# Optimization experiments

Measured on AMD Instinct MI355X. Metric: run time of the kernel, lower is better.

Reference implementation:

```python
import jax, jax.numpy as jnp
import numpy as np

T, B = 512, 256
OBS, ACT, HID, HF = 128, 32, 512, 512
IN = OBS + ACT  # GRUCell input: stoch_dim + action_dim
LOG2PI = float(np.log(2.0 * np.pi))


def _lin(key, out_f, in_f):
    k1, k2 = jax.random.split(key)
    s = 1.0 / np.sqrt(in_f)
    w = jax.random.uniform(k1, (out_f, in_f), jnp.float32, -s, s)
    b = jax.random.uniform(k2, (out_f,), jnp.float32, -s, s)
    return w, b


def setup_inputs() -> dict:
    key = jax.random.key(0)
    ks = jax.random.split(key, 16)
    obs = jax.random.normal(ks[0], (T, B, OBS), jnp.float32)
    action = jax.random.normal(ks[1], (T, B, ACT), jnp.float32)
    reward = jax.random.normal(ks[2], (T, B, 1), jnp.float32)
    w_ih, b_ih = _lin(ks[3], 3 * HID, IN)
    w_hh, b_hh = _lin(ks[4], 3 * HID, HID)
    ow0, ob0 = _lin(ks[5], HF, HID); ow1, ob1 = _lin(ks[6], HF, HF); ow2, ob2 = _lin(ks[7], OBS, HF)
    aw0, ab0 = _lin(ks[8], HF, HID); aw1, ab1 = _lin(ks[9], HF, HF); aw2, ab2 = _lin(ks[10], ACT, HF)
    rw0, rb0 = _lin(ks[11], HF, HID); rw1, rb1 = _lin(ks[12], HF, HF); rw2, rb2 = _lin(ks[13], 1, HF)
    return dict(obs=obs, action=action, reward=reward,
                w_ih=w_ih, w_hh=w_hh, b_ih=b_ih, b_hh=b_hh,
                ow0=ow0, ob0=ob0, ow1=ow1, ob1=ob1, ow2=ow2, ob2=ob2,
                aw0=aw0, ab0=ab0, aw1=aw1, ab1=ab1, aw2=aw2, ab2=ab2,
                rw0=rw0, rb0=rb0, rw1=rw1, rb1=rb1, rw2=rw2, rb2=rb2)


def _gru(x, h, w_ih, w_hh, b_ih, b_hh):
    # PyTorch GRUCell math
    gi = x @ w_ih.T + b_ih
    gh = h @ w_hh.T + b_hh
    ir, iz, inn = jnp.split(gi, 3, axis=-1)
    hr, hz, hn = jnp.split(gh, 3, axis=-1)
    r = jax.nn.sigmoid(ir + hr)
    z = jax.nn.sigmoid(iz + hz)
    n = jnp.tanh(inn + r * hn)
    return (1.0 - z) * n + z * h


def _mlp(x, w0, b0, w1, b1, w2, b2):
    x = jax.nn.elu(x @ w0.T + b0)
    x = jax.nn.elu(x @ w1.T + b1)
    return x @ w2.T + b2


def _logprob(x, mu):
    # Normal(mu, 1).log_prob(x)
    return -0.5 * (x - mu) ** 2 - 0.5 * LOG2PI


def reference(obs, action, reward,
              w_ih, w_hh, b_ih, b_hh,
              ow0, ob0, ow1, ob1, ow2, ob2,
              aw0, ab0, aw1, ab1, aw2, ab2,
              rw0, rb0, rw1, rb1, rw2, rb2):
    # initial h: GRUCell(cat([obs[0], zeros]), h=0)
    x0 = jnp.concatenate([obs[0], jnp.zeros_like(action[0])], axis=-1)
    h0 = _gru(x0, jnp.zeros((B, HID), obs.dtype), w_ih, w_hh, b_ih, b_hh)
    xseq = jnp.concatenate([obs, action], axis=-1)  # [T, B, IN]

    def step(h, x):
        return _gru(x, h, w_ih, w_hh, b_ih, b_hh), h  # emit h BEFORE update

    _, hs = jax.lax.scan(step, h0, xseq)  # hs[i] = hidden used at step i, [T, B, HID]

    pre_obs = _mlp(hs, ow0, ob0, ow1, ob1, ow2, ob2)  # [T, B, OBS]
    obs_loss = -jnp.sum(_logprob(obs, pre_obs)) / (T * B)

    pre_action = _mlp(jax.lax.stop_gradient(hs), aw0, ab0, aw1, ab1, aw2, ab2)  # [T, B, ACT]
    action_loss = -jnp.sum(_logprob(action, pre_action)) / (T * B)

    pre_reward = _mlp(hs, rw0, rb0, rw1, rb1, rw2, rb2)  # [T, B, 1]
    # NOTE: faithful to original bug: reward_dis.log_prob(_action), broadcasting [T,B,1] vs [T,B,ACT]
    reward_loss = -jnp.sum(_logprob(action, pre_reward)) / (T * B)

    loss = obs_loss + action_loss + reward_loss
    return loss, pre_obs, pre_action, pre_reward
```

## Files before the change

kernel.cpp:

```cpp
#include <hip/hip_runtime.h>
#include <math.h>

#define TT 512
#define BB 256
#define OBS 128
#define ACT 32
#define HID 512
#define AUX_SC 0x11

typedef unsigned short u16;
typedef unsigned int u32;
typedef __attribute__((ext_vector_type(8))) short bf16x8;
typedef __attribute__((ext_vector_type(4))) float f32x4;

__device__ __forceinline__ u16 f2bf(float v) {
  u32 u = __float_as_uint(v);
  u = (u + 0x7fff + ((u >> 16) & 1)) >> 16;
  return (u16)u;
}

__device__ __forceinline__ float fast_sigmoid(float x) {
  return 1.f / (1.f + __expf(-x));
}
__device__ __forceinline__ float fast_tanh(float x) {
  float e = __expf(-2.f * fabsf(x));
  float t = (1.f - e) / (1.f + e);
  return copysignf(t, x);
}


__global__ void k_init(double* acc, int* bars, u32* zb) {
  int tid = threadIdx.x;
  if (tid == 0) acc[0] = 0.0;
  for (int i = tid; i < 512; i += 256) bars[i * 16] = 0;
  zb[tid] = 0;
}

__global__ void k_convert_pad(const float* __restrict__ src, u16* __restrict__ dst,
                              int M, int K, int Mp, int Kp) {
  const int n = Mp * Kp;
  for (int idx = blockIdx.x * blockDim.x + threadIdx.x; idx < n;
       idx += gridDim.x * blockDim.x) {
    int m = idx / Kp, k = idx - m * Kp;
    float v = (m < M && k < K) ? src[(size_t)m * K + k] : 0.f;
    dst[idx] = f2bf(v);
  }
}

__global__ void k_prep_w(const float* __restrict__ w_ih, const float* __restrict__ w_hh,
                         const float* __restrict__ b_ih, const float* __restrict__ b_hh,
                         u16* __restrict__ Wr, u16* __restrict__ Wz,
                         u16* __restrict__ Wnh, u16* __restrict__ Wni,
                         float* __restrict__ bias4) {
  const int stride = gridDim.x * blockDim.x;
  const int t0 = blockIdx.x * blockDim.x + threadIdx.x;
  for (int idx = t0; idx < 512 * 704; idx += stride) {
    int j = idx / 704, k = idx - j * 704;
    float vr, vz;
    if (k < 512)      { vr = w_hh[(size_t)j * 512 + k];        vz = w_hh[(size_t)(512 + j) * 512 + k]; }
    else if (k < 672) { vr = w_ih[(size_t)j * 160 + (k - 512)]; vz = w_ih[(size_t)(512 + j) * 160 + (k - 512)]; }
    else              { vr = 0.f; vz = 0.f; }
    Wr[idx] = f2bf(vr); Wz[idx] = f2bf(vz);
  }
  for (int idx = t0; idx < 512 * 512; idx += stride) {
    int j = idx >> 9, k = idx & 511;
    Wnh[idx] = f2bf(w_hh[(size_t)(1024 + j) * 512 + k]);
  }
  for (int idx = t0; idx < 512 * 192; idx += stride) {
    int j = idx / 192, k = idx - j * 192;
    Wni[idx] = f2bf(k < 160 ? w_ih[(size_t)(1024 + j) * 160 + k] : 0.f);
  }
  for (int idx = t0; idx < 2048; idx += stride) {
    int g = idx >> 9, j = idx & 511;
    float v = (g == 0) ? b_ih[j] + b_hh[j]
            : (g == 1) ? b_ih[512 + j] + b_hh[512 + j]
            : (g == 2) ? b_ih[1024 + j] : b_hh[1024 + j];
    bias4[idx] = v;
  }
}

__global__ void k_pack_x(const float* __restrict__ obs, const float* __restrict__ action,
                         u16* __restrict__ Xb) {
  const int n = TT * BB * 160;
  for (int idx = blockIdx.x * blockDim.x + threadIdx.x; idx < n;
       idx += gridDim.x * blockDim.x) {
    int rr = idx / 160, cc = idx - rr * 160;
    int t = rr / BB, b = rr - t * BB;
    float v;
    if (t == 0) v = (cc < OBS) ? obs[(size_t)b * OBS + cc] : 0.f;
    else        v = (cc < OBS) ? obs[((size_t)(t - 1) * BB + b) * OBS + cc]
                               : action[((size_t)(t - 1) * BB + b) * ACT + (cc - OBS)];
    Xb[idx] = f2bf(v);
  }
}

__global__ __launch_bounds__(256, 2) void k_gru_seq(
    const u16* __restrict__ Wr, const u16* __restrict__ Wz,
    const u16* __restrict__ Wnh, const u16* __restrict__ Wni,
    const float* __restrict__ bias4, const u16* __restrict__ Xb,
    u16* __restrict__ hs,
    float* __restrict__ h32c,
    const u16* __restrict__ zb,
    int* __restrict__ bars,
    int t0, int TC)
{
  __shared__ __align__(16) u16 SB[40448];
  const int jt = blockIdx.x, bt = blockIdx.y;
  const int tid = threadIdx.x, w = tid >> 6, lane = tid & 63;
  const int m16 = lane & 15, q = lane >> 4;

  for (int i = w; i < 63; i += 4) {
    const u16* g;
    if (i < 48) {
      int gi = i >> 4, jj = i & 15;
      int c = lane ^ (jj & 7);
      int gjr = jt * 16 + jj;
      g = (gi == 0) ? Wr  + (size_t)gjr * 704 + c * 8
        : (gi == 1) ? Wz  + (size_t)gjr * 704 + c * 8
                    : Wnh + (size_t)gjr * 512 + c * 8;
    } else {
      int e = (i - 48) * 64 + lane;
      int gi = e / 320, rem = e - gi * 320;
      int jj = rem / 20, p = rem - jj * 20;
      int c = p - jj; if (c < 0) c += 20;
      int gjr = jt * 16 + jj;
      g = (gi == 0) ? Wni + (size_t)gjr * 192 + c * 8
        : (gi == 1) ? Wr  + (size_t)gjr * 704 + 512 + c * 8
                    : Wz  + (size_t)gjr * 704 + 512 + c * 8;
    }
    __builtin_amdgcn_global_load_lds((const __attribute__((address_space(1))) u32*)g,
        (__attribute__((address_space(3))) u32*)(SB + i * 512), 16, 0, 0);
  }

  u32 aoff[4];
#pragma unroll
  for (int n = 0; n < 4; ++n) {
    int i = w * 4 + n;
    aoff[n] = (u32)(bt * 16 + i) * 512 + (u32)(lane ^ (i & 7)) * 8;
  }

  const int eb = tid >> 4;
  const int ej = tid & 15;
  const int gj = jt * 16 + ej;
  const int gbrow = bt * 16 + eb;
  const float br = bias4[gj], bz = bias4[512 + gj];
  const float bi = bias4[1024 + gj], bh = bias4[1536 + gj];
  float hv = 0.f;
  if (t0 > 0) hv = h32c[(size_t)gbrow * 512 + gj];

  u16* As = SB + 32256;
  float* exch = (float*)(SB + 32256);
  const int myflag = (bt * 32 + jt) * 16;
  const int pollflag = (bt * 32 + (lane & 31)) * 16;

  for (int s = 0; s < TC; ++s) {
    const int t = t0 + s;
    const int sp = (s == 0) ? TC - 1 : s - 1;
    const u16* hsrc = hs + (size_t)sp * BB * 512;
    const u16* xsrc = Xb + (size_t)t * BB * 160;
    const bool hzero = (t == 0);

#pragma unroll
    for (int n = 0; n < 4; ++n) {
      const u16* g = hzero ? zb : hsrc + aoff[n];
      __builtin_amdgcn_global_load_lds((const __attribute__((address_space(1))) u32*)g,
          (__attribute__((address_space(3))) u32*)(As + (w * 4 + n) * 512), 16, 0, AUX_SC);
    }
    __syncthreads();

    f32x4 acc0 = (f32x4){0.f, 0.f, 0.f, 0.f};
    f32x4 acc1 = (f32x4){0.f, 0.f, 0.f, 0.f};
    f32x4 acc2 = (f32x4){0.f, 0.f, 0.f, 0.f};
    if (w < 3) {
      const int bbase = w * 8192;
#pragma unroll
      for (int ks = 0; ks < 16; ++ks) {
        int cb = ks * 4 + q;
        int sw = (cb ^ (m16 & 7)) * 8;
        bf16x8 af = *(const bf16x8*)&As[m16 * 512 + sw];
        bf16x8 bf = *(const bf16x8*)&SB[bbase + m16 * 512 + sw];
        acc0 = __builtin_amdgcn_mfma_f32_16x16x32_bf16(af, bf, acc0, 0, 0, 0);
      }
    } else {
#pragma unroll
      for (int ks = 0; ks < 5; ++ks) {
        int cb = ks * 4 + q;
        int pos = cb + m16; if (pos >= 20) pos -= 20;
        bf16x8 af = *(const bf16x8*)&xsrc[(size_t)(bt * 16 + m16) * 160 + cb * 8];
        bf16x8 b0 = *(const bf16x8*)&SB[24576 + m16 * 160 + pos * 8];
        bf16x8 b1 = *(const bf16x8*)&SB[27136 + m16 * 160 + pos * 8];
        bf16x8 b2 = *(const bf16x8*)&SB[29696 + m16 * 160 + pos * 8];
        acc0 = __builtin_amdgcn_mfma_f32_16x16x32_bf16(af, b0, acc0, 0, 0, 0);
        acc1 = __builtin_amdgcn_mfma_f32_16x16x32_bf16(af, b1, acc1, 0, 0, 0);
        acc2 = __builtin_amdgcn_mfma_f32_16x16x32_bf16(af, b2, acc2, 0, 0, 0);
      }
    }
    __syncthreads();

    if (w < 3) {
#pragma unroll
      for (int p = 0; p < 4; ++p)
        exch[w * 256 + (q * 4 + p) * 16 + m16] = acc0[p];
    } else {
#pragma unroll
      for (int p = 0; p < 4; ++p) {
        int o = (q * 4 + p) * 16 + m16;
        exch[768 + o]  = acc0[p];
        exch[1024 + o] = acc1[p];
        exch[1280 + o] = acc2[p];
      }
    }
    __syncthreads();

    {
      float rs  = exch[tid]        + exch[1024 + tid];
      float zs  = exch[256 + tid]  + exch[1280 + tid];
      float nhv = exch[512 + tid];
      float niv = exch[768 + tid];
      float r = fast_sigmoid(rs + br);
      float z = fast_sigmoid(zs + bz);
      float n = fast_tanh(niv + bi + r * (nhv + bh));
      float h = (1.f - z) * n + z * hv;
      hv = h;
      float ho = __shfl_xor(h, 1);
      if ((ej & 1) == 0) {
        u32 pk = (u32)f2bf(h) | ((u32)f2bf(ho) << 16);
        __hip_atomic_store((u32*)&hs[((size_t)s * BB + gbrow) * 512 + gj], pk,
                           __ATOMIC_RELAXED, __HIP_MEMORY_SCOPE_AGENT);
      }
    }

    __syncthreads();
    if (tid == 0)
      __hip_atomic_store(&bars[myflag], t + 1, __ATOMIC_RELAXED, __HIP_MEMORY_SCOPE_AGENT);
    if (w == 0) {
      int v = __hip_atomic_load(&bars[pollflag], __ATOMIC_RELAXED, __HIP_MEMORY_SCOPE_AGENT);
      while (__any(v < t + 1)) {
        __builtin_amdgcn_s_sleep(1);
        v = __hip_atomic_load(&bars[pollflag], __ATOMIC_RELAXED, __HIP_MEMORY_SCOPE_AGENT);
      }
    }
    __syncthreads();
  }

  h32c[(size_t)gbrow * 512 + gj] = hv;
}

__global__ __launch_bounds__(256) void k_mfma_gemm(
    const u16* __restrict__ A, const u16* __restrict__ B,
    const float* __restrict__ bias,
    float* __restrict__ outf, u16* __restrict__ outb,
    int N, int K, int M, int act)
{
  __shared__ u16 As[128 * 64];
  __shared__ u16 Bs[128 * 64];
  const int bn = blockIdx.y * 128;
  const int bm = blockIdx.x * 128;
  const int tid = threadIdx.x;
  const int w = tid >> 6, lane = tid & 63;
  const int wr = w >> 1, wc = w & 1;

  f32x4 acc[4][4];
#pragma unroll
  for (int i = 0; i < 4; ++i)
#pragma unroll
    for (int j = 0; j < 4; ++j) acc[i][j] = (f32x4){0.f, 0.f, 0.f, 0.f};

  const int lr8 = lane >> 3;
  const int lc8 = lane & 7;

  for (int kt = 0; kt < K; kt += 64) {
    __syncthreads();
#pragma unroll
    for (int i = 0; i < 4; ++i) {
      int r0 = (w * 4 + i) * 8;
      int r = r0 + lr8;
      int c = lc8 ^ (r & 7);
      const u16* ga = A + (size_t)(bn + r) * K + kt + c * 8;
      const u16* gb = B + (size_t)(bm + r) * K + kt + c * 8;
      __builtin_amdgcn_global_load_lds((const __attribute__((address_space(1))) u32*)ga,
                                       (__attribute__((address_space(3))) u32*)(As + r0 * 64), 16, 0, 0);
      __builtin_amdgcn_global_load_lds((const __attribute__((address_space(1))) u32*)gb,
                                       (__attribute__((address_space(3))) u32*)(Bs + r0 * 64), 16, 0, 0);
    }
    __syncthreads();

    const int m16 = lane & 15, q = lane >> 4;
#pragma unroll
    for (int kk = 0; kk < 2; ++kk) {
      bf16x8 af[4], bfr[4];
#pragma unroll
      for (int i = 0; i < 4; ++i) {
        int ra = wr * 64 + i * 16 + m16;
        af[i] = *(const bf16x8*)&As[ra * 64 + ((kk * 4 + q) ^ (ra & 7)) * 8];
        int rb = wc * 64 + i * 16 + m16;
        bfr[i] = *(const bf16x8*)&Bs[rb * 64 + ((kk * 4 + q) ^ (rb & 7)) * 8];
      }
#pragma unroll
      for (int i = 0; i < 4; ++i)
#pragma unroll
        for (int j = 0; j < 4; ++j)
          acc[i][j] = __builtin_amdgcn_mfma_f32_16x16x32_bf16(af[i], bfr[j], acc[i][j], 0, 0, 0);
    }
  }

  const int m16 = lane & 15, q = lane >> 4;
#pragma unroll
  for (int i = 0; i < 4; ++i) {
#pragma unroll
    for (int j = 0; j < 4; ++j) {
      int col = bm + wc * 64 + j * 16 + m16;
      if (col >= M) continue;
      float bs = bias[col];
#pragma unroll
      for (int p = 0; p < 4; ++p) {
        int row = bn + wr * 64 + i * 16 + q * 4 + p;
        float v = acc[i][j][p] + bs;
        if (act) v = (v > 0.f) ? v : (__expf(v) - 1.f);
        if (outf) outf[(size_t)row * M + col] = v;
        else      outb[(size_t)row * M + col] = f2bf(v);
      }
    }
  }
}

__global__ __launch_bounds__(256) void k_loss(
    const float* __restrict__ obs, const float* __restrict__ action,
    const float* __restrict__ p_obs, const float* __restrict__ p_act,
    const float* __restrict__ p_rew, double* __restrict__ acc)
{
  const long long n1 = (long long)TT * BB * OBS;
  const long long n2 = (long long)TT * BB * ACT;
  const long long n  = n1 + n2 + n2;
  const float C = 0.91893853320467274178f;
  double s = 0.0;
  for (long long idx = (long long)blockIdx.x * blockDim.x + threadIdx.x; idx < n;
       idx += (long long)gridDim.x * blockDim.x) {
    float d;
    if (idx < n1) {
      d = obs[idx] - p_obs[idx];
    } else if (idx < n1 + n2) {
      long long i = idx - n1;
      d = action[i] - p_act[i];
    } else {
      long long i = idx - n1 - n2;
      d = action[i] - p_rew[i >> 5];
    }
    s += (double)(0.5f * d * d + C);
  }
  __shared__ double red[256];
  red[threadIdx.x] = s;
  __syncthreads();
  for (int off = 128; off > 0; off >>= 1) {
    if ((int)threadIdx.x < off) red[threadIdx.x] += red[threadIdx.x + off];
    __syncthreads();
  }
  if (threadIdx.x == 0) atomicAdd(acc, red[0]);
}

__global__ void k_finalize(const double* __restrict__ acc, float* __restrict__ out) {
  if (threadIdx.x == 0) out[0] = (float)(acc[0] / (double)(TT * BB));
}


extern "C" void kernel_launch(void* const* d_in, const int* in_sizes, int n_in,
                              void* d_out, int out_size, void* d_ws, size_t ws_size,
                              hipStream_t stream) {
  const float* obs    = (const float*)d_in[0];
  const float* action = (const float*)d_in[1];
  const float* w_ih = (const float*)d_in[3];
  const float* w_hh = (const float*)d_in[4];
  const float* b_ih = (const float*)d_in[5];
  const float* b_hh = (const float*)d_in[6];
  const float* hw[9] = {(const float*)d_in[7],  (const float*)d_in[9],  (const float*)d_in[11],
                        (const float*)d_in[13], (const float*)d_in[15], (const float*)d_in[17],
                        (const float*)d_in[19], (const float*)d_in[21], (const float*)d_in[23]};
  const float* hb[9] = {(const float*)d_in[8],  (const float*)d_in[10], (const float*)d_in[12],
                        (const float*)d_in[14], (const float*)d_in[16], (const float*)d_in[18],
                        (const float*)d_in[20], (const float*)d_in[22], (const float*)d_in[24]};
  const int hM[9]  = {512, 512, 128, 512, 512, 32, 512, 512, 1};
  const int hMp[9] = {512, 512, 128, 512, 512, 128, 512, 512, 128};

  float* out     = (float*)d_out;
  float* pre_obs = out + 1;
  float* pre_act = pre_obs + (size_t)TT * BB * OBS;
  float* pre_rew = pre_act + (size_t)TT * BB * ACT;

  char* ws = (char*)d_ws;
  size_t off = 0;
  auto alloc = [&](size_t bytes) { void* p = ws + off; off = (off + bytes + 255) & ~(size_t)255; return p; };
  double* acc  = (double*)alloc(256);
  int* bars    = (int*)alloc(512 * 64);
  u32* zerobuf = (u32*)alloc(1024);
  u16* Wr  = (u16*)alloc((size_t)512 * 704 * 2);
  u16* Wz  = (u16*)alloc((size_t)512 * 704 * 2);
  u16* Wnh = (u16*)alloc((size_t)512 * 512 * 2);
  u16* Wni = (u16*)alloc((size_t)512 * 192 * 2);
  float* bias4 = (float*)alloc(2048 * 4);
  u16* headb[9];
  for (int i = 0; i < 9; ++i) headb[i] = (u16*)alloc((size_t)hMp[i] * 512 * 2);
  float* h32c = (float*)alloc((size_t)BB * 512 * 4);
  u16* Xb     = (u16*)alloc((size_t)TT * BB * 160 * 2);
  const size_t fixed = off;

  int TC = 512;
  while (TC > 8 && fixed + 3ull * TC * BB * 512 * 2ull + (1u << 20) > ws_size) TC >>= 1;
  u16* hs_chunk = (u16*)alloc((size_t)TC * BB * 512 * 2);
  u16* tmp1b    = (u16*)alloc((size_t)TC * BB * 512 * 2);
  u16* tmp2b    = (u16*)alloc((size_t)TC * BB * 512 * 2);
  const int CH = TC * BB;
  const int NCH = TT / TC;

  k_init<<<1, 256, 0, stream>>>(acc, bars, zerobuf);
  k_prep_w<<<512, 256, 0, stream>>>(w_ih, w_hh, b_ih, b_hh, Wr, Wz, Wnh, Wni, bias4);
  for (int i = 0; i < 9; ++i)
    k_convert_pad<<<512, 256, 0, stream>>>(hw[i], headb[i], hM[i], 512, hMp[i], 512);
  k_pack_x<<<4096, 256, 0, stream>>>(obs, action, Xb);

  for (int c = 0; c < NCH; ++c) {
    k_gru_seq<<<dim3(32, 16), 256, 0, stream>>>(
        Wr, Wz, Wnh, Wni, bias4, Xb, hs_chunk, h32c, (const u16*)zerobuf, bars, c * TC, TC);
    for (int h = 0; h < 3; ++h) {
      int M2 = hM[h * 3 + 2], Mp2 = hMp[h * 3 + 2];
      float* outp = (h == 0) ? pre_obs + (size_t)c * CH * OBS
                  : (h == 1) ? pre_act + (size_t)c * CH * ACT
                             : pre_rew + (size_t)c * CH;
      k_mfma_gemm<<<dim3(4, CH / 128), 256, 0, stream>>>(
          hs_chunk, headb[h * 3 + 0], hb[h * 3 + 0], nullptr, tmp1b, CH, 512, 512, 1);
      k_mfma_gemm<<<dim3(4, CH / 128), 256, 0, stream>>>(
          tmp1b, headb[h * 3 + 1], hb[h * 3 + 1], nullptr, tmp2b, CH, 512, 512, 1);
      k_mfma_gemm<<<dim3(Mp2 / 128, CH / 128), 256, 0, stream>>>(
          tmp2b, headb[h * 3 + 2], hb[h * 3 + 2], outp, nullptr, CH, 512, M2, 0);
    }
  }

  k_loss<<<2048, 256, 0, stream>>>(obs, action, pre_obs, pre_act, pre_rew, acc);
  k_finalize<<<1, 64, 0, stream>>>(acc, out);
}
```

Baseline: 2.956 ms.

## Keep GRU weights in registers and split batch into 8-row tiles across 1024 blocks

The persistent GRU kernel now holds each wave's weight fragments in registers instead of LDS and halves the batch tile per block from 16 to 8 rows, doubling the grid to 32x32 blocks with four blocks per CU. LDS shrinks to the hidden tile and exchange buffer, and one barrier after the MFMA loop is removed. The aim is to shorten per-step latency by spreading the recurrence over more CUs and cutting LDS traffic for weights. In exchange, half of each 16-row MFMA is wasted on padding rows, more blocks take part in the cross-block flag synchronisation, and register pressure rises. Dropping the barrier before writes to the exchange buffer may also be unsafe: exch occupies part of the same LDS as the previous region, which is not obviously disjoint from As, though As now ends at 8192.

Measured after the change: 3.268 ms. 1.11x slower.

```diff
diff --git a/kernel.cpp b/kernel.cpp
--- a/kernel.cpp
+++ b/kernel.cpp
@@ -32,7 +32,7 @@
 __global__ void k_init(double* acc, int* bars, u32* zb) {
   int tid = threadIdx.x;
   if (tid == 0) acc[0] = 0.0;
-  for (int i = tid; i < 512; i += 256) bars[i * 16] = 0;
+  for (int i = tid; i < 1024; i += 256) bars[i * 16] = 0;
   zb[tid] = 0;
 }
 
@@ -94,7 +94,7 @@
   }
 }
 
-__global__ __launch_bounds__(256, 2) void k_gru_seq(
+__global__ __launch_bounds__(256, 4) void k_gru_seq(
     const u16* __restrict__ Wr, const u16* __restrict__ Wz,
     const u16* __restrict__ Wnh, const u16* __restrict__ Wni,
     const float* __restrict__ bias4, const u16* __restrict__ Xb,
@@ -104,52 +104,56 @@
     int* __restrict__ bars,
     int t0, int TC)
 {
-  __shared__ __align__(16) u16 SB[40448];
+  __shared__ __align__(16) u16 SB[11264];
   const int jt = blockIdx.x, bt = blockIdx.y;
   const int tid = threadIdx.x, w = tid >> 6, lane = tid & 63;
   const int m16 = lane & 15, q = lane >> 4;
 
-  for (int i = w; i < 63; i += 4) {
-    const u16* g;
-    if (i < 48) {
-      int gi = i >> 4, jj = i & 15;
-      int c = lane ^ (jj & 7);
-      int gjr = jt * 16 + jj;
-      g = (gi == 0) ? Wr  + (size_t)gjr * 704 + c * 8
-        : (gi == 1) ? Wz  + (size_t)gjr * 704 + c * 8
-                    : Wnh + (size_t)gjr * 512 + c * 8;
+  bf16x8 wf[16];
+#pragma unroll
+  for (int i = 0; i < 16; ++i) wf[i] = (bf16x8){0, 0, 0, 0, 0, 0, 0, 0};
+  {
+    const int jr = jt * 16 + m16;
+    if (w < 3) {
+      const u16* Wg = (w == 0) ? Wr : (w == 1) ? Wz : Wnh;
+      const int ws_ = (w == 2) ? 512 : 704;
+#pragma unroll
+      for (int ks = 0; ks < 16; ++ks)
+        wf[ks] = *(const bf16x8*)&Wg[(size_t)jr * ws_ + (ks * 4 + q) * 8];
     } else {
-      int e = (i - 48) * 64 + lane;
-      int gi = e / 320, rem = e - gi * 320;
-      int jj = rem / 20, p = rem - jj * 20;
-      int c = p - jj; if (c < 0) c += 20;
-      int gjr = jt * 16 + jj;
-      g = (gi == 0) ? Wni + (size_t)gjr * 192 + c * 8
-        : (gi == 1) ? Wr  + (size_t)gjr * 704 + 512 + c * 8
-                    : Wz  + (size_t)gjr * 704 + 512 + c * 8;
-    }
-    __builtin_amdgcn_global_load_lds((const __attribute__((address_space(1))) u32*)g,
-        (__attribute__((address_space(3))) u32*)(SB + i * 512), 16, 0, 0);
-  }
-
-  u32 aoff[4];
-#pragma unroll
-  for (int n = 0; n < 4; ++n) {
-    int i = w * 4 + n;
-    aoff[n] = (u32)(bt * 16 + i) * 512 + (u32)(lane ^ (i & 7)) * 8;
-  }
+#pragma unroll
+      for (int ks = 0; ks < 5; ++ks) {
+        int cb = ks * 4 + q;
+        wf[ks * 3 + 0] = *(const bf16x8*)&Wni[(size_t)jr * 192 + cb * 8];
+        wf[ks * 3 + 1] = *(const bf16x8*)&Wr[(size_t)jr * 704 + 512 + cb * 8];
+        wf[ks * 3 + 2] = *(const bf16x8*)&Wz[(size_t)jr * 704 + 512 + cb * 8];
+      }
+    }
+  }
+
+  u32 aoff[2];
+#pragma unroll
+  for (int n = 0; n < 2; ++n) {
+    int i = w * 2 + n;
+    aoff[n] = (u32)(bt * 8 + i) * 512 + (u32)(lane ^ (i & 7)) * 8;
+  }
+
+  int xr = bt * 8 + m16;
+  if (xr > 255) xr = 255;
 
   const int eb = tid >> 4;
   const int ej = tid & 15;
   const int gj = jt * 16 + ej;
-  const int gbrow = bt * 16 + eb;
-  const float br = bias4[gj], bz = bias4[512 + gj];
-  const float bi = bias4[1024 + gj], bh = bias4[1536 + gj];
-  float hv = 0.f;
-  if (t0 > 0) hv = h32c[(size_t)gbrow * 512 + gj];
-
-  u16* As = SB + 32256;
-  float* exch = (float*)(SB + 32256);
+  const int gbrow = bt * 8 + eb;
+  const bool own = (tid < 128);
+  float br = 0.f, bz = 0.f, bi = 0.f, bh = 0.f, hv = 0.f;
+  if (own) {
+    br = bias4[gj]; bz = bias4[512 + gj]; bi = bias4[1024 + gj]; bh = bias4[1536 + gj];
+    if (t0 > 0) hv = h32c[(size_t)gbrow * 512 + gj];
+  }
+
+  u16* As = SB;
+  float* exch = (float*)(SB + 8192);
   const int myflag = (bt * 32 + jt) * 16;
   const int pollflag = (bt * 32 + (lane & 31)) * 16;
 
@@ -161,10 +165,10 @@
     const bool hzero = (t == 0);
 
 #pragma unroll
-    for (int n = 0; n < 4; ++n) {
+    for (int n = 0; n < 2; ++n) {
       const u16* g = hzero ? zb : hsrc + aoff[n];
       __builtin_amdgcn_global_load_lds((const __attribute__((address_space(1))) u32*)g,
-          (__attribute__((address_space(3))) u32*)(As + (w * 4 + n) * 512), 16, 0, AUX_SC);
+          (__attribute__((address_space(3))) u32*)(As + (w * 2 + n) * 512), 16, 0, AUX_SC);
     }
     __syncthreads();
 
@@ -172,30 +176,22 @@
     f32x4 acc1 = (f32x4){0.f, 0.f, 0.f, 0.f};
     f32x4 acc2 = (f32x4){0.f, 0.f, 0.f, 0.f};
     if (w < 3) {
-      const int bbase = w * 8192;
 #pragma unroll
       for (int ks = 0; ks < 16; ++ks) {
         int cb = ks * 4 + q;
-        int sw = (cb ^ (m16 & 7)) * 8;
-        bf16x8 af = *(const bf16x8*)&As[m16 * 512 + sw];
-        bf16x8 bf = *(const bf16x8*)&SB[bbase + m16 * 512 + sw];
-        acc0 = __builtin_amdgcn_mfma_f32_16x16x32_bf16(af, bf, acc0, 0, 0, 0);
+        bf16x8 af = *(const bf16x8*)&As[m16 * 512 + (cb ^ (m16 & 7)) * 8];
+        acc0 = __builtin_amdgcn_mfma_f32_16x16x32_bf16(af, wf[ks], acc0, 0, 0, 0);
       }
     } else {
 #pragma unroll
       for (int ks = 0; ks < 5; ++ks) {
         int cb = ks * 4 + q;
-        int pos = cb + m16; if (pos >= 20) pos -= 20;
-        bf16x8 af = *(const bf16x8*)&xsrc[(size_t)(bt * 16 + m16) * 160 + cb * 8];
-        bf16x8 b0 = *(const bf16x8*)&SB[24576 + m16 * 160 + pos * 8];
-        bf16x8 b1 = *(const bf16x8*)&SB[27136 + m16 * 160 + pos * 8];
-        bf16x8 b2 = *(const bf16x8*)&SB[29696 + m16 * 160 + pos * 8];
-        acc0 = __builtin_amdgcn_mfma_f32_16x16x32_bf16(af, b0, acc0, 0, 0, 0);
-        acc1 = __builtin_amdgcn_mfma_f32_16x16x32_bf16(af, b1, acc1, 0, 0, 0);
-        acc2 = __builtin_amdgcn_mfma_f32_16x16x32_bf16(af, b2, acc2, 0, 0, 0);
-      }
-    }
-    __syncthreads();
+        bf16x8 af = *(const bf16x8*)&xsrc[(size_t)xr * 160 + cb * 8];
+        acc0 = __builtin_amdgcn_mfma_f32_16x16x32_bf16(af, wf[ks * 3 + 0], acc0, 0, 0, 0);
+        acc1 = __builtin_amdgcn_mfma_f32_16x16x32_bf16(af, wf[ks * 3 + 1], acc1, 0, 0, 0);
+        acc2 = __builtin_amdgcn_mfma_f32_16x16x32_bf16(af, wf[ks * 3 + 2], acc2, 0, 0, 0);
+      }
+    }
 
     if (w < 3) {
 #pragma unroll
@@ -212,7 +208,7 @@
     }
     __syncthreads();
 
-    {
+    if (own) {
       float rs  = exch[tid]        + exch[1024 + tid];
       float zs  = exch[256 + tid]  + exch[1280 + tid];
       float nhv = exch[512 + tid];
@@ -243,7 +239,7 @@
     __syncthreads();
   }
 
-  h32c[(size_t)gbrow * 512 + gj] = hv;
+  if (own) h32c[(size_t)gbrow * 512 + gj] = hv;
 }
 
 __global__ __launch_bounds__(256) void k_mfma_gemm(
@@ -390,7 +386,7 @@
   size_t off = 0;
   auto alloc = [&](size_t bytes) { void* p = ws + off; off = (off + bytes + 255) & ~(size_t)255; return p; };
   double* acc  = (double*)alloc(256);
-  int* bars    = (int*)alloc(512 * 64);
+  int* bars    = (int*)alloc(1024 * 64);
   u32* zerobuf = (u32*)alloc(1024);
   u16* Wr  = (u16*)alloc((size_t)512 * 704 * 2);
   u16* Wz  = (u16*)alloc((size_t)512 * 704 * 2);
@@ -418,7 +414,7 @@
   k_pack_x<<<4096, 256, 0, stream>>>(obs, action, Xb);
 
   for (int c = 0; c < NCH; ++c) {
-    k_gru_seq<<<dim3(32, 16), 256, 0, stream>>>(
+    k_gru_seq<<<dim3(32, 32), 256, 0, stream>>>(
         Wr, Wz, Wnh, Wni, bias4, Xb, hs_chunk, h32c, (const u16*)zerobuf, bars, c * TC, TC);
     for (int h = 0; h < 3; ++h) {
       int M2 = hM[h * 3 + 2], Mp2 = hMp[h * 3 + 2];
```
